# Performance work log

Hardware: AMD Instinct MI355X
Metric: run time of the kernel (lower is better)

## Reference

```python
import jax, jax.numpy as jnp
import numpy as np

B, S, D = 2, 2048, 2048
H, HKV, HD = 32, 8, 64          # query heads, kv heads, head dim (GQA factor 4)
WIN = 1024                       # sliding_window_length
QKV_DIM = HD * (H + 2 * HKV)     # 3072


def setup_inputs() -> dict:
    key = jax.random.key(0)
    k0, k1, k2, k3, k4 = jax.random.split(key, 5)
    x = jax.random.normal(k0, (B, S, D), dtype=jnp.float32)
    Wqkv = jax.random.normal(k1, (QKV_DIM, D), dtype=jnp.float32) * 0.02
    bqkv = jax.random.normal(k2, (QKV_DIM,), dtype=jnp.float32) * 0.02
    Wout = jax.random.normal(k3, (D, H * HD), dtype=jnp.float32) * 0.02
    bout = jax.random.normal(k4, (D,), dtype=jnp.float32) * 0.02
    return {"x": x, "Wqkv": Wqkv, "bqkv": bqkv, "Wout": Wout, "bout": bout}


def reference(x, Wqkv, bqkv, Wout, bout):
    rep = H // HKV
    scale = 1.0 / np.sqrt(HD).astype(np.float32)
    # in_proj (torch Linear: y = x @ W.T + b)
    qkv = jnp.einsum('bsd,ed->bse', x, Wqkv) + bqkv          # [B,S,QKV_DIM]
    q = qkv[..., : H * HD].reshape(B, S, HKV, rep, HD)        # grouped query heads
    kv = qkv[..., H * HD:].reshape(B, S, 2, HKV, HD)
    k, v = kv[:, :, 0], kv[:, :, 1]                           # [B,S,HKV,HD]
    # GQA attention without materializing repeated K/V: group query heads per kv head
    scores = jnp.einsum('bqgrd,bkgd->bgrqk', q, k) * scale    # [B,HKV,rep,S,S]
    i = jnp.arange(S)[:, None]
    j = jnp.arange(S)[None, :]
    mask = (j <= i) & (j > i - WIN)
    scores = jnp.where(mask, scores, -jnp.inf)
    attn = jax.nn.softmax(scores, axis=-1)
    ctx = jnp.einsum('bgrqk,bkgd->bqgrd', attn, v)            # [B,S,HKV,rep,HD]
    ctx = ctx.reshape(B, S, H * HD)
    out = jnp.einsum('bse,de->bsd', ctx, Wout) + bout
    return out
```

## Files before the change

### kernel.cpp

```cpp
#include <hip/hip_runtime.h>
#include <stdint.h>

#define S_LEN   2048
#define D_MODEL 2048
#define NH      32
#define NKV     8
#define HDIM    64
#define WIN     1024
#define QKV_N   3072
#define MTOT    4096
#define QSCALE  0.18033688011112042f

typedef __bf16 bf16x8 __attribute__((ext_vector_type(8)));
typedef float  f32x4  __attribute__((ext_vector_type(4)));
typedef unsigned short u16x8 __attribute__((ext_vector_type(8)));
typedef unsigned short u16x4 __attribute__((ext_vector_type(4)));

#define GLDS16(g, l) __builtin_amdgcn_global_load_lds( \
    (__attribute__((address_space(1))) void*)(g),      \
    (__attribute__((address_space(3))) void*)(l), 16, 0, 0)

__device__ __forceinline__ unsigned short f2bf(float f) {
  __bf16 b = (__bf16)f;
  return __builtin_bit_cast(unsigned short, b);
}

__global__ void cvt3(const float* __restrict__ s0, unsigned short* __restrict__ d0, int n0,
                     const float* __restrict__ s1, unsigned short* __restrict__ d1, int n1,
                     const float* __restrict__ s2, unsigned short* __restrict__ d2, int n2)
{
  int total4 = (n0 + n1 + n2) >> 2;
  for (int idx = blockIdx.x * blockDim.x + threadIdx.x; idx < total4;
       idx += gridDim.x * blockDim.x) {
    int i = idx << 2;
    const float* s; unsigned short* d;
    if (i < n0)            { s = s0 + i;            d = d0 + i; }
    else if (i < n0 + n1)  { s = s1 + (i - n0);     d = d1 + (i - n0); }
    else                   { s = s2 + (i - n0 - n1); d = d2 + (i - n0 - n1); }
    float4 v = *(const float4*)s;
    u16x4 o;
    o[0] = f2bf(v.x); o[1] = f2bf(v.y); o[2] = f2bf(v.z); o[3] = f2bf(v.w);
    *(u16x4*)d = o;
  }
}

template<int EP>
__global__ __launch_bounds__(256)
void gemm_nt(const unsigned short* __restrict__ A, const unsigned short* __restrict__ Bm,
             const float* __restrict__ bias, int K, int N,
             unsigned short* __restrict__ qo, unsigned short* __restrict__ ko,
             unsigned short* __restrict__ vo, float* __restrict__ co)
{
  __shared__ unsigned short sA[128 * 32];
  __shared__ unsigned short sB[128 * 32];
  const int t = threadIdx.x;
  const int l = t & 63;
  const int brow = blockIdx.y << 7;
  const int bcol = blockIdx.x << 7;
  const int wr = ((t >> 7) & 1) << 6;
  const int wc = ((t >> 6) & 1) << 6;

  const int srow  = t >> 2;
  const int skoff = (t & 3) << 3;
  const unsigned short* aP = A + (size_t)(brow + srow) * K + skoff;
  const unsigned short* bP = Bm + (size_t)(bcol + srow) * K + skoff;
  unsigned short* ldsA0 = &sA[(t & 192) << 3];
  unsigned short* ldsA1 = &sA[(256 + (t & 192)) << 3];
  unsigned short* ldsB0 = &sB[(t & 192) << 3];
  unsigned short* ldsB1 = &sB[(256 + (t & 192)) << 3];

  f32x4 acc[4][4] = {};
  const int fr = l & 15;
  const int fk = (l >> 4) << 3;

  for (int kt = 0; kt < K; kt += 32) {
    GLDS16(aP, ldsA0);
    GLDS16(aP + (size_t)64 * K, ldsA1);
    GLDS16(bP, ldsB0);
    GLDS16(bP + (size_t)64 * K, ldsB1);
    aP += 32; bP += 32;
    __syncthreads();

    bf16x8 af[4], bf[4];
#pragma unroll
    for (int mi = 0; mi < 4; ++mi)
      af[mi] = *(const bf16x8*)&sA[(wr + mi * 16 + fr) * 32 + fk];
#pragma unroll
    for (int ni = 0; ni < 4; ++ni)
      bf[ni] = *(const bf16x8*)&sB[(wc + ni * 16 + fr) * 32 + fk];
#pragma unroll
    for (int mi = 0; mi < 4; ++mi)
#pragma unroll
      for (int ni = 0; ni < 4; ++ni)
        acc[mi][ni] = __builtin_amdgcn_mfma_f32_16x16x32_bf16(af[mi], bf[ni], acc[mi][ni], 0, 0, 0);
    __syncthreads();
  }

  const int fq4 = (l >> 4) << 2;
  if (EP == 0) {
#pragma unroll
    for (int ni = 0; ni < 4; ++ni) {
      const int e = bcol + wc + ni * 16 + fr;
      const float bs = bias[e];
#pragma unroll
      for (int mi = 0; mi < 4; ++mi) {
#pragma unroll
        for (int j = 0; j < 4; ++j) {
          const int m = brow + wr + mi * 16 + fq4 + j;
          const int b = m >> 11, s = m & 2047;
          float v = acc[mi][ni][j] + bs;
          const int d = e & 63;
          if (e < 2048) {
            const int h = e >> 6;
            qo[(((size_t)b * NH + h) * S_LEN + s) * HDIM + d] = f2bf(v * QSCALE);
          } else if (e < 2560) {
            const int gg = (e - 2048) >> 6;
            ko[(((size_t)b * NKV + gg) * S_LEN + s) * HDIM + d] = f2bf(v);
          } else {
            const int gg = (e - 2560) >> 6;
            vo[(((size_t)b * NKV + gg) * HDIM + d) * S_LEN + s] = f2bf(v);
          }
        }
      }
    }
  } else {
#pragma unroll
    for (int mi = 0; mi < 4; ++mi)
#pragma unroll
      for (int j = 0; j < 4; ++j) {
        const int m = brow + wr + mi * 16 + fq4 + j;
#pragma unroll
        for (int ni = 0; ni < 4; ++ni) {
          const int n = bcol + wc + ni * 16 + fr;
          co[(size_t)m * N + n] = acc[mi][ni][j] + bias[n];
        }
      }
  }
}

__global__ __launch_bounds__(512)
void attn_swin(const unsigned short* __restrict__ Qs, const unsigned short* __restrict__ Kb,
               const unsigned short* __restrict__ Vtb, unsigned short* __restrict__ ctx)
{
  __shared__ char lds[32768];

  const int t = threadIdx.x, w = t >> 6, l = t & 63;
  const int fr = l & 15, fq = l >> 4;
  const int qh = w & 3, kh = w >> 2;
  const int q0 = blockIdx.x << 6;
  const int h = blockIdx.y, b = blockIdx.z;
  const int g = h >> 2;

  const unsigned short* qp = Qs + (((size_t)(b * NH + h)) * S_LEN + q0 + (qh << 4)) * HDIM;
  const bf16x8 qf0 = *(const bf16x8*)(qp + fr * HDIM + (fq << 3));
  const bf16x8 qf1 = *(const bf16x8*)(qp + fr * HDIM + 32 + (fq << 3));

  const unsigned short* Kg  = Kb  + ((size_t)(b * NKV + g)) * S_LEN * HDIM;
  const unsigned short* Vtg = Vtb + ((size_t)(b * NKV + g)) * HDIM * S_LEN;

  float m_run = -1e30f, l_part = 0.0f;
  f32x4 o_acc[4] = {};

  int lo = q0 - (WIN - 1); if (lo < 0) lo = 0; lo &= ~63;
  const int hi = q0 + 64;
  const int full_lo = q0 - (WIN - 64);
  const int full_hi = q0 - 64;

  const unsigned short* src0;
  const unsigned short* src1;
  {
    const int x0 = ((w & 3) << 11) + (l << 4);
    const int x1 = x0 + 1024;
    if (w < 4) {
      const int s0 = x0 >> 7, o0 = ((x0 >> 4) & 7) ^ (s0 & 7);
      const int s1 = x1 >> 7, o1 = ((x1 >> 4) & 7) ^ (s1 & 7);
      const int p0 = ((s0 >> 5) << 5) | (((s0 >> 2) & 3) << 3) | (((s0 >> 4) & 1) << 2) | (s0 & 3);
      const int p1 = ((s1 >> 5) << 5) | (((s1 >> 2) & 3) << 3) | (((s1 >> 4) & 1) << 2) | (s1 & 3);
      src0 = Kg + (size_t)(lo + p0) * HDIM + (o0 << 3);
      src1 = Kg + (size_t)(lo + p1) * HDIM + (o1 << 3);
    } else {
      const int d0 = x0 >> 7, o0 = ((x0 >> 4) & 7) ^ (d0 & 7);
      const int d1 = x1 >> 7, o1 = ((x1 >> 4) & 7) ^ (d1 & 7);
      src0 = Vtg + (size_t)d0 * S_LEN + lo + (o0 << 3);
      src1 = Vtg + (size_t)d1 * S_LEN + lo + (o1 << 3);
    }
  }
  const int sadv = (w < 4) ? 64 * HDIM : 64;
  const int dbase = ((w < 4) ? 0 : 8192) + ((w & 3) << 11) + (l << 4);

  char* bufA = lds;
  char* bufB = lds + 16384;

  GLDS16(src0, bufA + dbase);
  GLDS16(src1, bufA + dbase + 1024);
  src0 += sadv; src1 += sadv;

  const int iq = q0 + (qh << 4) + fr;
  const int swr = (fr & 7) << 4;

  auto TILE = [&](int kv0, const char* sK, const char* sV, bool MASKED)
      __attribute__((always_inline)) {
    bf16x8 kf[2][2];
#pragma unroll
    for (int ntg = 0; ntg < 2; ++ntg) {
      const int slot = (kh << 5) + (ntg << 4) + fr;
      kf[ntg][0] = *(const bf16x8*)(sK + (((slot << 7) + (fq << 4)) ^ swr));
      kf[ntg][1] = *(const bf16x8*)(sK + (((slot << 7) + ((fq + 4) << 4)) ^ swr));
    }
    __builtin_amdgcn_s_setprio(1);
    f32x4 sf[2];
#pragma unroll
    for (int ntg = 0; ntg < 2; ++ntg) {
      f32x4 z = {};
      z = __builtin_amdgcn_mfma_f32_16x16x32_bf16(kf[ntg][0], qf0, z, 0, 0, 0);
      z = __builtin_amdgcn_mfma_f32_16x16x32_bf16(kf[ntg][1], qf1, z, 0, 0, 0);
      sf[ntg] = z;
    }
    __builtin_amdgcn_s_setprio(0);
    if (MASKED) {
#pragma unroll
      for (int ntg = 0; ntg < 2; ++ntg)
#pragma unroll
        for (int r = 0; r < 4; ++r) {
          const int jk = kv0 + (kh << 5) + (fq << 3) + (ntg << 2) + r;
          if (jk > iq || jk <= iq - WIN) sf[ntg][r] = -1e30f;
        }
    }
    float pmax;
    {
      f32x4 mx = sf[0];
      mx[0] = fmaxf(mx[0], sf[1][0]); mx[1] = fmaxf(mx[1], sf[1][1]);
      mx[2] = fmaxf(mx[2], sf[1][2]); mx[3] = fmaxf(mx[3], sf[1][3]);
      pmax = fmaxf(fmaxf(mx[0], mx[1]), fmaxf(mx[2], mx[3]));
    }
    if (__any(pmax - m_run > 8.0f)) {
      float rmax = fmaxf(pmax, __shfl_xor(pmax, 16));
      rmax = fmaxf(rmax, __shfl_xor(rmax, 32));
      const float mnew = fmaxf(m_run, rmax);
      const float rs = exp2f(m_run - mnew);
      m_run = mnew;
      l_part *= rs;
      float rs_o[4];
#pragma unroll
      for (int r = 0; r < 4; ++r) rs_o[r] = __shfl(rs, (fq << 2) + r, 16);
#pragma unroll
      for (int dt = 0; dt < 4; ++dt)
#pragma unroll
        for (int r = 0; r < 4; ++r) o_acc[dt][r] *= rs_o[r];
    }
    union { unsigned short us[8]; bf16x8 v; } pu;
    float lloc = 0.0f;
#pragma unroll
    for (int ntg = 0; ntg < 2; ++ntg)
#pragma unroll
      for (int r = 0; r < 4; ++r) {
        const float p = exp2f(sf[ntg][r] - m_run);
        lloc += p;
        pu.us[(ntg << 2) + r] = f2bf(p);
      }
    l_part += lloc;
    bf16x8 vf[4];
#pragma unroll
    for (int dt = 0; dt < 4; ++dt) {
      const int d = (dt << 4) + fr;
      vf[dt] = *(const bf16x8*)(sV + ((d << 7) + ((((kh << 2) + fq) ^ (fr & 7)) << 4)));
    }
    __builtin_amdgcn_s_setprio(1);
#pragma unroll
    for (int dt = 0; dt < 4; ++dt)
      o_acc[dt] = __builtin_amdgcn_mfma_f32_16x16x32_bf16(pu.v, vf[dt], o_acc[dt], 0, 0, 0);
    __builtin_amdgcn_s_setprio(0);
  };

  for (int kv0 = lo; kv0 < hi; kv0 += 64) {
    __syncthreads();
    if (kv0 + 64 < hi) {
      GLDS16(src0, bufB + dbase);
      GLDS16(src1, bufB + dbase + 1024);
      src0 += sadv; src1 += sadv;
    }
    const bool masked = (kv0 < full_lo) || (kv0 > full_hi);
    if (masked) TILE(kv0, bufA, bufA + 8192, true);
    else        TILE(kv0, bufA, bufA + 8192, false);
    char* tmp = bufA; bufA = bufB; bufB = tmp;
  }

  float lsum = l_part;
  lsum += __shfl_xor(lsum, 16);
  lsum += __shfl_xor(lsum, 32);

  __syncthreads();
  if (w < 4) {
    char* ob = lds + ((w & 3) << 12);
#pragma unroll
    for (int dt = 0; dt < 4; ++dt)
      *(f32x4*)(ob + (dt << 10) + (l << 4)) = o_acc[dt];
    if (fq == 0) {
      *(float*)(lds + 16384 + ((w & 3) << 7) + (fr << 3))     = m_run;
      *(float*)(lds + 16384 + ((w & 3) << 7) + (fr << 3) + 4) = lsum;
    }
  }
  __syncthreads();
  if (w >= 4) {
    const char* ob = lds + ((w & 3) << 12);
    const float m_p = *(const float*)(lds + 16384 + ((w & 3) << 7) + (fr << 3));
    const float l_p = *(const float*)(lds + 16384 + ((w & 3) << 7) + (fr << 3) + 4);
    const float m_f = fmaxf(m_run, m_p);
    const float a  = exp2f(m_run - m_f);
    const float bb = exp2f(m_p  - m_f);
    const float inv = 1.0f / (a * lsum + bb * l_p);
    const float alpha = a * inv, beta = bb * inv;
    float al[4], be[4];
#pragma unroll
    for (int r = 0; r < 4; ++r) {
      al[r] = __shfl(alpha, (fq << 2) + r, 16);
      be[r] = __shfl(beta,  (fq << 2) + r, 16);
    }
    unsigned short* cp = ctx + ((size_t)(b * S_LEN + q0 + (qh << 4))) * D_MODEL + h * HDIM;
#pragma unroll
    for (int dt = 0; dt < 4; ++dt) {
      const f32x4 op = *(const f32x4*)(ob + (dt << 10) + (l << 4));
#pragma unroll
      for (int r = 0; r < 4; ++r) {
        const float of = al[r] * o_acc[dt][r] + be[r] * op[r];
        cp[(size_t)((fq << 2) + r) * D_MODEL + (dt << 4) + fr] = f2bf(of);
      }
    }
  }
}

extern "C" void kernel_launch(void* const* d_in, const int* in_sizes, int n_in,
                              void* d_out, int out_size, void* d_ws, size_t ws_size,
                              hipStream_t stream)
{
  const float* x    = (const float*)d_in[0];
  const float* Wqkv = (const float*)d_in[1];
  const float* bqkv = (const float*)d_in[2];
  const float* Wout = (const float*)d_in[3];
  const float* bout = (const float*)d_in[4];
  float* out = (float*)d_out;

  char* ws = (char*)d_ws;
  if (ws_size < 62914560u) return;

  unsigned short* xb    = (unsigned short*)(ws);
  unsigned short* ctx   = xb;
  unsigned short* wqkvb = (unsigned short*)(ws + 16777216);
  unsigned short* woutb = (unsigned short*)(ws + 29360128);
  unsigned short* Qs    = (unsigned short*)(ws + 37748736);
  unsigned short* Kbuf  = (unsigned short*)(ws + 54525952);
  unsigned short* Vtbuf = (unsigned short*)(ws + 58720256);

  cvt3<<<2048, 256, 0, stream>>>(x, xb, MTOT * D_MODEL,
                                 Wqkv, wqkvb, QKV_N * D_MODEL,
                                 Wout, woutb, D_MODEL * D_MODEL);

  gemm_nt<0><<<dim3(QKV_N / 128, MTOT / 128), 256, 0, stream>>>(
      xb, wqkvb, bqkv, D_MODEL, QKV_N, Qs, Kbuf, Vtbuf, nullptr);

  attn_swin<<<dim3(S_LEN / 64, NH, 2), 512, 0, stream>>>(Qs, Kbuf, Vtbuf, ctx);

  gemm_nt<1><<<dim3(D_MODEL / 128, MTOT / 128), 256, 0, stream>>>(
      ctx, woutb, bout, D_MODEL, D_MODEL, nullptr, nullptr, nullptr, out);
}
```

Baseline: 224.7 us.

## Switch attention to 32x32x16 MFMA with 128-query blocks

The sliding-window attention kernel moves from 16x16x32 to 32x32x16 bf16 MFMA. Each block now handles 128 queries instead of 64, with each wave owning 32 query rows, which halves the number of K/V tile loads per query and the grid size. K and V LDS layouts and swizzles are remapped to the 32-wide fragment layout, and the softmax and merge bookkeeping are rewritten for 16-element accumulators. The risks are fewer blocks to fill the GPU, more masked work at the band edges, and higher register pressure.

```diff
diff --git a/kernel.cpp b/kernel.cpp
--- a/kernel.cpp
+++ b/kernel.cpp
@@ -13,6 +13,7 @@
 
 typedef __bf16 bf16x8 __attribute__((ext_vector_type(8)));
 typedef float  f32x4  __attribute__((ext_vector_type(4)));
+typedef float  f32x16 __attribute__((ext_vector_type(16)));
 typedef unsigned short u16x8 __attribute__((ext_vector_type(8)));
 typedef unsigned short u16x4 __attribute__((ext_vector_type(4)));
 
@@ -142,28 +143,30 @@
 void attn_swin(const unsigned short* __restrict__ Qs, const unsigned short* __restrict__ Kb,
                const unsigned short* __restrict__ Vtb, unsigned short* __restrict__ ctx)
 {
-  __shared__ char lds[32768];
+  __shared__ char lds[34816];
 
   const int t = threadIdx.x, w = t >> 6, l = t & 63;
-  const int fr = l & 15, fq = l >> 4;
+  const int lq = l & 31, hi = l >> 5;
   const int qh = w & 3, kh = w >> 2;
-  const int q0 = blockIdx.x << 6;
+  const int q0 = blockIdx.x << 7;
   const int h = blockIdx.y, b = blockIdx.z;
   const int g = h >> 2;
 
-  const unsigned short* qp = Qs + (((size_t)(b * NH + h)) * S_LEN + q0 + (qh << 4)) * HDIM;
-  const bf16x8 qf0 = *(const bf16x8*)(qp + fr * HDIM + (fq << 3));
-  const bf16x8 qf1 = *(const bf16x8*)(qp + fr * HDIM + 32 + (fq << 3));
+  const unsigned short* qp = Qs + (((size_t)(b * NH + h)) * S_LEN + q0 + (qh << 5) + lq) * HDIM;
+  bf16x8 qf[4];
+#pragma unroll
+  for (int c = 0; c < 4; ++c)
+    qf[c] = *(const bf16x8*)(qp + (c << 4) + (hi << 3));
 
   const unsigned short* Kg  = Kb  + ((size_t)(b * NKV + g)) * S_LEN * HDIM;
   const unsigned short* Vtg = Vtb + ((size_t)(b * NKV + g)) * HDIM * S_LEN;
 
   float m_run = -1e30f, l_part = 0.0f;
-  f32x4 o_acc[4] = {};
+  f32x16 o_acc[2] = {};
 
   int lo = q0 - (WIN - 1); if (lo < 0) lo = 0; lo &= ~63;
-  const int hi = q0 + 64;
-  const int full_lo = q0 - (WIN - 64);
+  const int hi2 = q0 + 128;
+  const int full_lo = q0 - (WIN - 128);
   const int full_hi = q0 - 64;
 
   const unsigned short* src0;
@@ -172,17 +175,20 @@
     const int x0 = ((w & 3) << 11) + (l << 4);
     const int x1 = x0 + 1024;
     if (w < 4) {
-      const int s0 = x0 >> 7, o0 = ((x0 >> 4) & 7) ^ (s0 & 7);
-      const int s1 = x1 >> 7, o1 = ((x1 >> 4) & 7) ^ (s1 & 7);
-      const int p0 = ((s0 >> 5) << 5) | (((s0 >> 2) & 3) << 3) | (((s0 >> 4) & 1) << 2) | (s0 & 3);
-      const int p1 = ((s1 >> 5) << 5) | (((s1 >> 2) & 3) << 3) | (((s1 >> 4) & 1) << 2) | (s1 & 3);
-      src0 = Kg + (size_t)(lo + p0) * HDIM + (o0 << 3);
-      src1 = Kg + (size_t)(lo + p1) * HDIM + (o1 << 3);
+      const int s0 = x0 >> 7, sl0 = s0 & 31;
+      const int s1 = x1 >> 7, sl1 = s1 & 31;
+      const int p0 = ((s0 >> 5) << 5) + (sl0 & 16) + ((sl0 & 4) << 1) + ((sl0 & 8) >> 1) + (sl0 & 3);
+      const int p1 = ((s1 >> 5) << 5) + (sl1 & 16) + ((sl1 & 4) << 1) + ((sl1 & 8) >> 1) + (sl1 & 3);
+      const int o0 = (x0 & 127) ^ ((s0 & 7) << 4);
+      const int o1 = (x1 & 127) ^ ((s1 & 7) << 4);
+      src0 = Kg + (size_t)(lo + p0) * HDIM + (o0 >> 1);
+      src1 = Kg + (size_t)(lo + p1) * HDIM + (o1 >> 1);
     } else {
-      const int d0 = x0 >> 7, o0 = ((x0 >> 4) & 7) ^ (d0 & 7);
-      const int d1 = x1 >> 7, o1 = ((x1 >> 4) & 7) ^ (d1 & 7);
-      src0 = Vtg + (size_t)d0 * S_LEN + lo + (o0 << 3);
-      src1 = Vtg + (size_t)d1 * S_LEN + lo + (o1 << 3);
+      const int d0 = x0 >> 7, d1 = x1 >> 7;
+      const int o0 = (x0 & 127) ^ ((d0 & 7) << 4);
+      const int o1 = (x1 & 127) ^ ((d1 & 7) << 4);
+      src0 = Vtg + (size_t)d0 * S_LEN + lo + (o0 >> 1);
+      src1 = Vtg + (size_t)d1 * S_LEN + lo + (o1 >> 1);
     }
   }
   const int sadv = (w < 4) ? 64 * HDIM : 64;
@@ -195,86 +201,79 @@
   GLDS16(src1, bufA + dbase + 1024);
   src0 += sadv; src1 += sadv;
 
-  const int iq = q0 + (qh << 4) + fr;
-  const int swr = (fr & 7) << 4;
+  const int iq = q0 + (qh << 5) + lq;
+  const int swz = (lq & 7) << 4;
+  const int kbase = (((kh << 5) + lq) << 7) + (hi << 4);
 
   auto TILE = [&](int kv0, const char* sK, const char* sV, bool MASKED)
       __attribute__((always_inline)) {
-    bf16x8 kf[2][2];
-#pragma unroll
-    for (int ntg = 0; ntg < 2; ++ntg) {
-      const int slot = (kh << 5) + (ntg << 4) + fr;
-      kf[ntg][0] = *(const bf16x8*)(sK + (((slot << 7) + (fq << 4)) ^ swr));
-      kf[ntg][1] = *(const bf16x8*)(sK + (((slot << 7) + ((fq + 4) << 4)) ^ swr));
-    }
+    bf16x8 kf[4];
+#pragma unroll
+    for (int c = 0; c < 4; ++c)
+      kf[c] = *(const bf16x8*)(sK + ((kbase + (c << 5)) ^ swz));
     __builtin_amdgcn_s_setprio(1);
-    f32x4 sf[2];
-#pragma unroll
-    for (int ntg = 0; ntg < 2; ++ntg) {
-      f32x4 z = {};
-      z = __builtin_amdgcn_mfma_f32_16x16x32_bf16(kf[ntg][0], qf0, z, 0, 0, 0);
-      z = __builtin_amdgcn_mfma_f32_16x16x32_bf16(kf[ntg][1], qf1, z, 0, 0, 0);
-      sf[ntg] = z;
-    }
+    f32x16 sf = {};
+#pragma unroll
+    for (int c = 0; c < 4; ++c)
+      sf = __builtin_amdgcn_mfma_f32_32x32x16_bf16(kf[c], qf[c], sf, 0, 0, 0);
     __builtin_amdgcn_s_setprio(0);
     if (MASKED) {
 #pragma unroll
-      for (int ntg = 0; ntg < 2; ++ntg)
-#pragma unroll
-        for (int r = 0; r < 4; ++r) {
-          const int jk = kv0 + (kh << 5) + (fq << 3) + (ntg << 2) + r;
-          if (jk > iq || jk <= iq - WIN) sf[ntg][r] = -1e30f;
-        }
-    }
-    float pmax;
-    {
-      f32x4 mx = sf[0];
-      mx[0] = fmaxf(mx[0], sf[1][0]); mx[1] = fmaxf(mx[1], sf[1][1]);
-      mx[2] = fmaxf(mx[2], sf[1][2]); mx[3] = fmaxf(mx[3], sf[1][3]);
-      pmax = fmaxf(fmaxf(mx[0], mx[1]), fmaxf(mx[2], mx[3]));
-    }
+      for (int r = 0; r < 16; ++r) {
+        const int jk = kv0 + (kh << 5) + ((r >> 3) << 4) + (hi << 3) + (r & 7);
+        if (jk > iq || jk <= iq - WIN) sf[r] = -1e30f;
+      }
+    }
+    float m0 = fmaxf(sf[0], sf[8]),  m1_ = fmaxf(sf[1], sf[9]);
+    float m2 = fmaxf(sf[2], sf[10]), m3 = fmaxf(sf[3], sf[11]);
+    float m4 = fmaxf(sf[4], sf[12]), m5 = fmaxf(sf[5], sf[13]);
+    float m6 = fmaxf(sf[6], sf[14]), m7 = fmaxf(sf[7], sf[15]);
+    m0 = fmaxf(m0, m4); m1_ = fmaxf(m1_, m5); m2 = fmaxf(m2, m6); m3 = fmaxf(m3, m7);
+    const float pmax = fmaxf(fmaxf(m0, m1_), fmaxf(m2, m3));
     if (__any(pmax - m_run > 8.0f)) {
-      float rmax = fmaxf(pmax, __shfl_xor(pmax, 16));
-      rmax = fmaxf(rmax, __shfl_xor(rmax, 32));
+      float rmax = fmaxf(pmax, __shfl_xor(pmax, 32));
       const float mnew = fmaxf(m_run, rmax);
       const float rs = exp2f(m_run - mnew);
       m_run = mnew;
       l_part *= rs;
-      float rs_o[4];
-#pragma unroll
-      for (int r = 0; r < 4; ++r) rs_o[r] = __shfl(rs, (fq << 2) + r, 16);
-#pragma unroll
-      for (int dt = 0; dt < 4; ++dt)
-#pragma unroll
-        for (int r = 0; r < 4; ++r) o_acc[dt][r] *= rs_o[r];
-    }
-    union { unsigned short us[8]; bf16x8 v; } pu;
+#pragma unroll
+      for (int r = 0; r < 16; ++r) {
+        const float rr = __shfl(rs, (r & 3) + ((r >> 2) << 3) + (hi << 2), 32);
+        o_acc[0][r] *= rr;
+        o_acc[1][r] *= rr;
+      }
+    }
+    union { unsigned short us[8]; bf16x8 v; } pu[2];
     float lloc = 0.0f;
 #pragma unroll
-    for (int ntg = 0; ntg < 2; ++ntg)
-#pragma unroll
-      for (int r = 0; r < 4; ++r) {
-        const float p = exp2f(sf[ntg][r] - m_run);
+    for (int m1 = 0; m1 < 2; ++m1)
+#pragma unroll
+      for (int e = 0; e < 8; ++e) {
+        const float p = exp2f(sf[(m1 << 3) + e] - m_run);
         lloc += p;
-        pu.us[(ntg << 2) + r] = f2bf(p);
+        pu[m1].us[e] = f2bf(p);
       }
     l_part += lloc;
-    bf16x8 vf[4];
-#pragma unroll
-    for (int dt = 0; dt < 4; ++dt) {
-      const int d = (dt << 4) + fr;
-      vf[dt] = *(const bf16x8*)(sV + ((d << 7) + ((((kh << 2) + fq) ^ (fr & 7)) << 4)));
-    }
+    bf16x8 vf[2][2];
+#pragma unroll
+    for (int m1 = 0; m1 < 2; ++m1)
+#pragma unroll
+      for (int dt = 0; dt < 2; ++dt) {
+        const int base = (((dt << 5) + lq) << 7) + (kh << 6) + (m1 << 5) + (hi << 4);
+        vf[m1][dt] = *(const bf16x8*)(sV + (base ^ swz));
+      }
     __builtin_amdgcn_s_setprio(1);
 #pragma unroll
-    for (int dt = 0; dt < 4; ++dt)
-      o_acc[dt] = __builtin_amdgcn_mfma_f32_16x16x32_bf16(pu.v, vf[dt], o_acc[dt], 0, 0, 0);
+    for (int dt = 0; dt < 2; ++dt)
+#pragma unroll
+      for (int m1 = 0; m1 < 2; ++m1)
+        o_acc[dt] = __builtin_amdgcn_mfma_f32_32x32x16_bf16(pu[m1].v, vf[m1][dt], o_acc[dt], 0, 0, 0);
     __builtin_amdgcn_s_setprio(0);
   };
 
-  for (int kv0 = lo; kv0 < hi; kv0 += 64) {
+  for (int kv0 = lo; kv0 < hi2; kv0 += 64) {
     __syncthreads();
-    if (kv0 + 64 < hi) {
+    if (kv0 + 64 < hi2) {
       GLDS16(src0, bufB + dbase);
       GLDS16(src1, bufB + dbase + 1024);
       src0 += sadv; src1 += sadv;
@@ -285,45 +284,48 @@
     char* tmp = bufA; bufA = bufB; bufB = tmp;
   }
 
-  float lsum = l_part;
-  lsum += __shfl_xor(lsum, 16);
-  lsum += __shfl_xor(lsum, 32);
+  const float lsum = l_part + __shfl_xor(l_part, 32);
 
   __syncthreads();
   if (w < 4) {
-    char* ob = lds + ((w & 3) << 12);
-#pragma unroll
-    for (int dt = 0; dt < 4; ++dt)
-      *(f32x4*)(ob + (dt << 10) + (l << 4)) = o_acc[dt];
-    if (fq == 0) {
-      *(float*)(lds + 16384 + ((w & 3) << 7) + (fr << 3))     = m_run;
-      *(float*)(lds + 16384 + ((w & 3) << 7) + (fr << 3) + 4) = lsum;
+    char* ob = lds + (qh << 13);
+#pragma unroll
+    for (int dt = 0; dt < 2; ++dt)
+#pragma unroll
+      for (int j = 0; j < 4; ++j) {
+        f32x4 s4 = { o_acc[dt][4*j], o_acc[dt][4*j+1], o_acc[dt][4*j+2], o_acc[dt][4*j+3] };
+        *(f32x4*)(ob + (dt << 12) + (l << 6) + (j << 4)) = s4;
+      }
+    if (hi == 0) {
+      *(float*)(lds + 32768 + (qh << 8) + (lq << 3))     = m_run;
+      *(float*)(lds + 32768 + (qh << 8) + (lq << 3) + 4) = lsum;
     }
   }
   __syncthreads();
   if (w >= 4) {
-    const char* ob = lds + ((w & 3) << 12);
-    const float m_p = *(const float*)(lds + 16384 + ((w & 3) << 7) + (fr << 3));
-    const float l_p = *(const float*)(lds + 16384 + ((w & 3) << 7) + (fr << 3) + 4);
+    const char* ob = lds + (qh << 13);
+    const float m_p = *(const float*)(lds + 32768 + (qh << 8) + (lq << 3));
+    const float l_p = *(const float*)(lds + 32768 + (qh << 8) + (lq << 3) + 4);
     const float m_f = fmaxf(m_run, m_p);
     const float a  = exp2f(m_run - m_f);
     const float bb = exp2f(m_p  - m_f);
     const float inv = 1.0f / (a * lsum + bb * l_p);
     const float alpha = a * inv, beta = bb * inv;
-    float al[4], be[4];
-#pragma unroll
-    for (int r = 0; r < 4; ++r) {
-      al[r] = __shfl(alpha, (fq << 2) + r, 16);
-      be[r] = __shfl(beta,  (fq << 2) + r, 16);
-    }
-    unsigned short* cp = ctx + ((size_t)(b * S_LEN + q0 + (qh << 4))) * D_MODEL + h * HDIM;
-#pragma unroll
-    for (int dt = 0; dt < 4; ++dt) {
-      const f32x4 op = *(const f32x4*)(ob + (dt << 10) + (l << 4));
-#pragma unroll
-      for (int r = 0; r < 4; ++r) {
-        const float of = al[r] * o_acc[dt][r] + be[r] * op[r];
-        cp[(size_t)((fq << 2) + r) * D_MODEL + (dt << 4) + fr] = f2bf(of);
+    unsigned short* cp = ctx + ((size_t)(b * S_LEN + q0 + (qh << 5))) * D_MODEL + h * HDIM;
+#pragma unroll
+    for (int dt = 0; dt < 2; ++dt) {
+#pragma unroll
+      for (int j = 0; j < 4; ++j) {
+        const f32x4 op = *(const f32x4*)(ob + (dt << 12) + (l << 6) + (j << 4));
+#pragma unroll
+        for (int k = 0; k < 4; ++k) {
+          const int r = 4*j + k;
+          const int qq = (r & 3) + ((r >> 2) << 3) + (hi << 2);
+          const float al = __shfl(alpha, qq, 32);
+          const float be = __shfl(beta,  qq, 32);
+          const float of = al * o_acc[dt][r] + be * op[k];
+          cp[(size_t)qq * D_MODEL + (dt << 5) + lq] = f2bf(of);
+        }
       }
     }
   }
@@ -358,7 +360,7 @@
   gemm_nt<0><<<dim3(QKV_N / 128, MTOT / 128), 256, 0, stream>>>(
       xb, wqkvb, bqkv, D_MODEL, QKV_N, Qs, Kbuf, Vtbuf, nullptr);
 
-  attn_swin<<<dim3(S_LEN / 64, NH, 2), 512, 0, stream>>>(Qs, Kbuf, Vtbuf, ctx);
+  attn_swin<<<dim3(S_LEN / 128, NH, 2), 512, 0, stream>>>(Qs, Kbuf, Vtbuf, ctx);
 
   gemm_nt<1><<<dim3(D_MODEL / 128, MTOT / 128), 256, 0, stream>>>(
       ctx, woutb, bout, D_MODEL, D_MODEL, nullptr, nullptr, nullptr, out);
```

Result: slower. 242.3 us (+7.8%).

## Replace QKV projection GEMM with 256x256 tile, 8-wave, 4-stage pipelined kernel

Applied to the files above, without the earlier changes.

Adds a new QKV projection GEMM that computes 256x256 output tiles with 512 threads (8 waves, 2x4 layout). It streams A and B through a 4-stage LDS ring of 64-byte K chunks using global_load_lds, issuing the next loads between MFMA phases and synchronising with explicit barriers, vmcnt waits and setprio. The goal is to hide global-memory latency and raise MFMA utilisation over the old single-buffered 128x128 kernel. In exchange it needs 128KB of dynamic LDS, which limits occupancy to one block per CU, and the grid shrinks to 12x16 = 192 blocks, which may leave CUs idle and add tail effects.

```diff
diff --git a/kernel.cpp b/kernel.cpp
--- a/kernel.cpp
+++ b/kernel.cpp
@@ -23,6 +23,13 @@
 __device__ __forceinline__ unsigned short f2bf(float f) {
   __bf16 b = (__bf16)f;
   return __builtin_bit_cast(unsigned short, b);
+}
+
+__device__ __forceinline__ void hard_barrier() {
+  asm volatile("" ::: "memory");
+  __builtin_amdgcn_s_barrier();
+  asm volatile("" ::: "memory");
+  __builtin_amdgcn_sched_barrier(0);
 }
 
 __global__ void cvt3(const float* __restrict__ s0, unsigned short* __restrict__ d0, int n0,
@@ -44,6 +51,108 @@
   }
 }
 
+__global__ __launch_bounds__(512, 2)
+void gemm8p_qkv(const unsigned short* __restrict__ A, const unsigned short* __restrict__ Bm,
+                const float* __restrict__ bias,
+                unsigned short* __restrict__ qo, unsigned short* __restrict__ ko,
+                unsigned short* __restrict__ vo)
+{
+  extern __shared__ char lds[];
+  const int K2 = D_MODEL * 2;
+  const int t = threadIdx.x, w = t >> 6, l = t & 63;
+  const int fr = l & 15, fq = l >> 4;
+  const int wm = w >> 2, wn = w & 3;
+  const int bm0 = blockIdx.y << 8, bn0 = blockIdx.x << 8;
+
+  const int srow = t >> 2;
+  const int scol = (t & 3) << 4;
+  const char* aR0 = (const char*)A  + (size_t)(bm0 + srow) * K2 + scol;
+  const char* aR1 = aR0 + (size_t)128 * K2;
+  const char* bR0 = (const char*)Bm + (size_t)(bn0 + srow) * K2 + scol;
+  const char* bR1 = bR0 + (size_t)128 * K2;
+  char* ldsW = lds + (w << 10);
+
+  f32x4 acc[8][4] = {};
+
+  GLDS16(aR0 + 0,   ldsW + 0);          GLDS16(aR1 + 0,   ldsW + 8192);
+  GLDS16(bR0 + 0,   ldsW + 65536);      GLDS16(bR1 + 0,   ldsW + 65536 + 8192);
+  GLDS16(aR0 + 64,  ldsW + 16384);      GLDS16(aR1 + 64,  ldsW + 16384 + 8192);
+  GLDS16(bR0 + 64,  ldsW + 81920);      GLDS16(bR1 + 64,  ldsW + 81920 + 8192);
+  GLDS16(aR0 + 128, ldsW + 32768);      GLDS16(aR1 + 128, ldsW + 32768 + 8192);
+  GLDS16(bR0 + 128, ldsW + 98304);      GLDS16(bR1 + 128, ldsW + 98304 + 8192);
+  asm volatile("s_waitcnt vmcnt(8)" ::: "memory");
+  hard_barrier();
+
+  bf16x8 afr[4], bfr[4];
+  constexpr int stBase[4] = { 49152, 0, 16384, 32768 };
+
+  for (int i = 0; i < 16; ++i) {
+    const int c0 = i << 8;
+#pragma unroll
+    for (int p = 0; p < 8; ++p) {
+      const int pr = p >> 1;
+      const int mh = p & 1;
+      const int aLr = ((pr >> 1) << 15) + ((pr & 1) << 14);
+      const int bLr = 65536 + aLr;
+      if (mh == 0) {
+#pragma unroll
+        for (int ni = 0; ni < 4; ++ni)
+          bfr[ni] = *(const bf16x8*)(lds + bLr +
+              (((wn << 6) + (ni << 4) + fr) << 6) + (fq << 4));
+      }
+#pragma unroll
+      for (int j = 0; j < 4; ++j)
+        afr[j] = *(const bf16x8*)(lds + aLr +
+            (((wm << 7) + (((mh << 2) + j) << 4) + fr) << 6) + (fq << 4));
+      {
+        const int coff = c0 + 192 + (pr << 6);
+        const int dst = stBase[pr] + (mh << 16);
+        const char* s0 = mh ? bR0 : aR0;
+        const char* s1 = mh ? bR1 : aR1;
+        GLDS16(s0 + coff, ldsW + dst);
+        GLDS16(s1 + coff, ldsW + dst + 8192);
+      }
+      hard_barrier();
+      __builtin_amdgcn_s_setprio(1);
+#pragma unroll
+      for (int j = 0; j < 4; ++j)
+#pragma unroll
+        for (int ni = 0; ni < 4; ++ni)
+          acc[(mh << 2) + j][ni] = __builtin_amdgcn_mfma_f32_16x16x32_bf16(
+              afr[j], bfr[ni], acc[(mh << 2) + j][ni], 0, 0, 0);
+      __builtin_amdgcn_s_setprio(0);
+      if (mh) asm volatile("s_waitcnt vmcnt(8)" ::: "memory");
+      hard_barrier();
+    }
+  }
+
+#pragma unroll
+  for (int ni = 0; ni < 4; ++ni) {
+    const int e = bn0 + (wn << 6) + (ni << 4) + fr;
+    const float bs = bias[e];
+    const int d = e & 63;
+#pragma unroll
+    for (int mi = 0; mi < 8; ++mi) {
+#pragma unroll
+      for (int j = 0; j < 4; ++j) {
+        const int m = bm0 + (wm << 7) + (mi << 4) + (fq << 2) + j;
+        const int b = m >> 11, s = m & 2047;
+        const float v = acc[mi][ni][j] + bs;
+        if (e < 2048) {
+          const int h = e >> 6;
+          qo[(((size_t)b * NH + h) * S_LEN + s) * HDIM + d] = f2bf(v * QSCALE);
+        } else if (e < 2560) {
+          const int gg = (e - 2048) >> 6;
+          ko[(((size_t)b * NKV + gg) * S_LEN + s) * HDIM + d] = f2bf(v);
+        } else {
+          const int gg = (e - 2560) >> 6;
+          vo[(((size_t)b * NKV + gg) * HDIM + d) * S_LEN + s] = f2bf(v);
+        }
+      }
+    }
+  }
+}
+
 template<int EP>
 __global__ __launch_bounds__(256)
 void gemm_nt(const unsigned short* __restrict__ A, const unsigned short* __restrict__ Bm,
@@ -97,33 +206,7 @@
   }
 
   const int fq4 = (l >> 4) << 2;
-  if (EP == 0) {
-#pragma unroll
-    for (int ni = 0; ni < 4; ++ni) {
-      const int e = bcol + wc + ni * 16 + fr;
-      const float bs = bias[e];
-#pragma unroll
-      for (int mi = 0; mi < 4; ++mi) {
-#pragma unroll
-        for (int j = 0; j < 4; ++j) {
-          const int m = brow + wr + mi * 16 + fq4 + j;
-          const int b = m >> 11, s = m & 2047;
-          float v = acc[mi][ni][j] + bs;
-          const int d = e & 63;
-          if (e < 2048) {
-            const int h = e >> 6;
-            qo[(((size_t)b * NH + h) * S_LEN + s) * HDIM + d] = f2bf(v * QSCALE);
-          } else if (e < 2560) {
-            const int gg = (e - 2048) >> 6;
-            ko[(((size_t)b * NKV + gg) * S_LEN + s) * HDIM + d] = f2bf(v);
-          } else {
-            const int gg = (e - 2560) >> 6;
-            vo[(((size_t)b * NKV + gg) * HDIM + d) * S_LEN + s] = f2bf(v);
-          }
-        }
-      }
-    }
-  } else {
+  if (EP == 1) {
 #pragma unroll
     for (int mi = 0; mi < 4; ++mi)
 #pragma unroll
@@ -351,12 +434,15 @@
   unsigned short* Kbuf  = (unsigned short*)(ws + 54525952);
   unsigned short* Vtbuf = (unsigned short*)(ws + 58720256);
 
+  (void)hipFuncSetAttribute((const void*)gemm8p_qkv,
+                            hipFuncAttributeMaxDynamicSharedMemorySize, 131072);
+
   cvt3<<<2048, 256, 0, stream>>>(x, xb, MTOT * D_MODEL,
                                  Wqkv, wqkvb, QKV_N * D_MODEL,
                                  Wout, woutb, D_MODEL * D_MODEL);
 
-  gemm_nt<0><<<dim3(QKV_N / 128, MTOT / 128), 256, 0, stream>>>(
-      xb, wqkvb, bqkv, D_MODEL, QKV_N, Qs, Kbuf, Vtbuf, nullptr);
+  gemm8p_qkv<<<dim3(QKV_N / 256, MTOT / 256), 512, 131072, stream>>>(
+      xb, wqkvb, bqkv, Qs, Kbuf, Vtbuf);
 
   attn_swin<<<dim3(S_LEN / 64, NH, 2), 512, 0, stream>>>(Qs, Kbuf, Vtbuf, ctx);
 
```

Result: slower. 231.7 us (+3.1%).
